# Optimization experiments

Measured on AMD Instinct MI355X. Metric: run time of the kernel, lower is better.

Reference implementation:

```python
import jax, jax.numpy as jnp
import numpy as np

B, S, H = 2, 2048, 4096
NH, HD = 32, 128          # num attention heads, head dim (kv_channels)
KVH = 2                   # multi_query_group_num (KV heads)
ROT = HD // 2             # 64 rotary dims -> rope cache last-2 dim = 32
QKV = NH * HD + 2 * KVH * HD  # 4608


def apply_rope(x, rope):
    # x: [b, nh, s, hd]; rope: [b, s, ROT//2, 2]
    b, nh, s, hd = x.shape
    x_rot, x_pass = x[..., :ROT], x[..., ROT:]
    xs = x_rot.reshape(b, nh, s, ROT // 2, 2)
    rc = rope[:, :s].reshape(b, 1, s, ROT // 2, 2)
    out = jnp.stack([
        xs[..., 0] * rc[..., 0] - xs[..., 1] * rc[..., 1],
        xs[..., 1] * rc[..., 0] + xs[..., 0] * rc[..., 1],
    ], axis=-1).reshape(b, nh, s, ROT)
    return jnp.concatenate([out, x_pass], axis=-1)


def setup_inputs() -> dict:
    key = jax.random.key(0)
    ks = jax.random.split(key, 6)
    hidden_states = jax.random.normal(ks[0], (B, S, H), dtype=jnp.float32)
    rotary_pos_emb = jax.random.normal(ks[1], (B, S, ROT // 2, 2), dtype=jnp.float32)
    # causal mask: True = masked (strict upper triangle), matching module's ~tril
    causal = jnp.triu(jnp.ones((S, S), dtype=jnp.bool_), k=1)
    attention_mask = jnp.broadcast_to(causal[None, None], (B, 1, S, S))
    W_qkv = jax.random.normal(ks[2], (QKV, H), dtype=jnp.float32) * (1.0 / np.sqrt(H))
    b_qkv = jax.random.normal(ks[3], (QKV,), dtype=jnp.float32) * 0.02
    W_dense = jax.random.normal(ks[4], (H, NH * HD), dtype=jnp.float32) * (1.0 / np.sqrt(NH * HD))
    return {"hidden_states": hidden_states, "rotary_pos_emb": rotary_pos_emb,
            "attention_mask": attention_mask, "W_qkv": W_qkv, "b_qkv": b_qkv,
            "W_dense": W_dense}


def reference(hidden_states, rotary_pos_emb, attention_mask, W_qkv, b_qkv, W_dense):
    b, s, _ = hidden_states.shape
    mixed = hidden_states @ W_qkv.T + b_qkv  # [b, s, QKV]
    q, k, v = jnp.split(mixed, [NH * HD, NH * HD + KVH * HD], axis=-1)
    q = q.reshape(b, s, NH, HD).transpose(0, 2, 1, 3)   # [b, NH, s, hd]
    k = k.reshape(b, s, KVH, HD).transpose(0, 2, 1, 3)  # [b, KVH, s, hd]
    v = v.reshape(b, s, KVH, HD).transpose(0, 2, 1, 3)
    q = apply_rope(q, rotary_pos_emb)
    k = apply_rope(k, rotary_pos_emb)
    # GQA expand KV heads to NH
    rep = NH // KVH
    k = jnp.repeat(k, rep, axis=1)
    v = jnp.repeat(v, rep, axis=1)
    scale = 1.0 / np.sqrt(HD)
    scores = jnp.einsum('bhqd,bhkd->bhqk', q, k).astype(jnp.float32) * scale
    scores = jnp.where(attention_mask, -jnp.inf, scores)
    probs = jax.nn.softmax(scores, axis=-1).astype(v.dtype)
    ctx = jnp.einsum('bhqk,bhkd->bhqd', probs, v)       # [b, NH, s, hd]
    ctx = ctx.transpose(0, 2, 1, 3).reshape(b, s, NH * HD)
    return ctx @ W_dense.T
```

## Files before the change

### kernel.cpp

```cpp
#include <hip/hip_runtime.h>
#include <hip/hip_bf16.h>
#include <stdint.h>

#define Bb 2
#define Ss 2048
#define Hh 4096
#define NHh 32
#define HDd 128
#define KVHh 2

typedef __attribute__((ext_vector_type(8))) short bf16x8;
typedef __attribute__((ext_vector_type(4))) float f32x4;
typedef __attribute__((ext_vector_type(16))) float f32x16;
typedef __attribute__((ext_vector_type(4))) unsigned int u32x4;
typedef unsigned short u16;
typedef unsigned int u32;
typedef unsigned long long u64;

__device__ __forceinline__ u16 f2b(float f) {
  union { float f; u32 u; } v; v.f = f;
  u32 r = v.u + 0x7fffu + ((v.u >> 16) & 1u);
  return (u16)(r >> 16);
}
__device__ __forceinline__ float b2f(u16 h) {
  union { u32 u; float f; } v; v.u = ((u32)h) << 16;
  return v.f;
}

__device__ __forceinline__ u32 cvtpk(float lo, float hi_) {
  u32 r;
  asm("v_cvt_pk_bf16_f32 %0, %1, %2" : "=v"(r) : "v"(lo), "v"(hi_));
  return r;
}
__device__ __forceinline__ void plswap(u32& x, u32& y) {
  asm volatile("v_permlane32_swap_b32 %0, %1" : "+v"(x), "+v"(y));
}

__device__ __forceinline__ void gload_lds16(const u16* g, u16* l) {
  __builtin_amdgcn_global_load_lds(
      (const __attribute__((address_space(1))) u32*)(uintptr_t)g,
      (__attribute__((address_space(3))) u32*)(u32)(uintptr_t)l,
      16, 0, 0);
}

__global__ void cvt_k(const float* __restrict__ in, u16* __restrict__ out, int n) {
  int i = blockIdx.x * blockDim.x + threadIdx.x;
  int idx = i * 4;
  if (idx >= n) return;
  float4 v = *(const float4*)&in[idx];
  u64 pack = (u64)f2b(v.x) | ((u64)f2b(v.y) << 16) |
             ((u64)f2b(v.z) << 32) | ((u64)f2b(v.w) << 48);
  *(u64*)&out[idx] = pack;
}

__global__ void rope_k(u16* __restrict__ X, const float* __restrict__ rope, int nheads) {
  int i = blockIdx.x * blockDim.x + threadIdx.x;
  int p = i & 31;
  int s = (i >> 5) & (Ss - 1);
  int bh = i >> 16;
  if (bh >= Bb * nheads) return;
  int b = bh / nheads;
  size_t base = ((size_t)bh * Ss + s) * HDd + p * 2;
  u32 x01 = *(u32*)&X[base];
  float x0 = b2f((u16)(x01 & 0xffff));
  float x1 = b2f((u16)(x01 >> 16));
  float2 rc = *(const float2*)&rope[(((size_t)b * Ss + s) * 32 + p) * 2];
  float o0 = x0 * rc.x - x1 * rc.y;
  float o1 = x1 * rc.x + x0 * rc.y;
  u32 o = (u32)f2b(o0) | ((u32)f2b(o1) << 16);
  *(u32*)&X[base] = o;
}

template <int KK>
__device__ __forceinline__ void stage_tileA(const u16* __restrict__ gbase, u16* dst, int tid) {
#pragma unroll
  for (int li = 0; li < 2; ++li) {
    int t16 = li * 512 + tid;
    int rt = t16 >> 2, ct = t16 & 3;
    int cg = ct ^ ((rt >> 1) & 3);
    gload_lds16(gbase + (size_t)rt * KK + cg * 8, dst + t16 * 8);
  }
}
template <int KK>
__device__ __forceinline__ void stage_tileB(const u16* __restrict__ gbase, u16* dst, int tid) {
  int t16 = tid;
  int rt = t16 >> 2, ct = t16 & 3;
  int cg = ct ^ ((rt >> 1) & 3);
  gload_lds16(gbase + (size_t)rt * KK + cg * 8, dst + t16 * 8);
}

__device__ __forceinline__ bf16x8 frag128(const u16* buf, int row, int lk) {
  int ch = lk ^ ((row >> 1) & 3);
  return *(const bf16x8*)&buf[row * 32 + ch * 8];
}

template <int NN, int KK, int COLG, int EPI>
__global__ __launch_bounds__(512, 4) void gemm256x128(
    const u16* __restrict__ A, const u16* __restrict__ Bm,
    float* __restrict__ Cout, const float* __restrict__ bias,
    u16* __restrict__ Qb, u16* __restrict__ Kb, u16* __restrict__ Vb) {
  __shared__ u16 As[2][8192];
  __shared__ u16 Bs[2][4096];
  const int tid = threadIdx.x;
  const int wave = tid >> 6;
  const int lane = tid & 63;
  const int lr = lane & 15;
  const int lk = lane >> 4;
  const int wr = wave >> 1;
  const int wc = wave & 1;
  const int bid = blockIdx.x;
  const int xcd = bid & 7;
  const int local = bid >> 3;
  const int rlr = local / COLG;
  const int rlc = local - rlr * COLG;
  const int m0 = ((xcd >> 2) * 8 + rlr) * 256;
  const int n0 = ((xcd & 3) * COLG + rlc) * 128;
  const int NT = KK / 32;

  f32x4 acc[4][4];
#pragma unroll
  for (int i = 0; i < 4; ++i)
#pragma unroll
    for (int j = 0; j < 4; ++j) acc[i][j] = (f32x4){0.f, 0.f, 0.f, 0.f};

  const u16* Ab = A + (size_t)m0 * KK;
  const u16* Bb_ = Bm + (size_t)n0 * KK;

  stage_tileA<KK>(Ab, &As[0][0], tid);
  stage_tileB<KK>(Bb_, &Bs[0][0], tid);
  asm volatile("s_waitcnt vmcnt(0)");
  __syncthreads();

  int cur = 0;
  for (int t = 0; t < NT; ++t) {
    if (t + 1 < NT) {
      stage_tileA<KK>(Ab + (t + 1) * 32, &As[cur ^ 1][0], tid);
      stage_tileB<KK>(Bb_ + (t + 1) * 32, &Bs[cur ^ 1][0], tid);
      asm volatile("s_waitcnt vmcnt(3)");
    } else {
      asm volatile("s_waitcnt vmcnt(0)");
    }
    __builtin_amdgcn_s_barrier();
    __builtin_amdgcn_sched_barrier(0);

    bf16x8 af[4], bf[4];
#pragma unroll
    for (int mi = 0; mi < 4; ++mi)
      af[mi] = frag128(&As[cur][0], wr * 64 + mi * 16 + lr, lk);
#pragma unroll
    for (int ni = 0; ni < 4; ++ni)
      bf[ni] = frag128(&Bs[cur][0], wc * 64 + ni * 16 + lr, lk);
    asm volatile("s_waitcnt lgkmcnt(0)");
    __builtin_amdgcn_sched_barrier(0);
    __builtin_amdgcn_s_setprio(1);
#pragma unroll
    for (int mi = 0; mi < 4; ++mi)
#pragma unroll
      for (int ni = 0; ni < 4; ++ni)
        acc[mi][ni] = __builtin_amdgcn_mfma_f32_16x16x32_bf16(af[mi], bf[ni], acc[mi][ni], 0, 0, 0);
    __builtin_amdgcn_s_setprio(0);
    __builtin_amdgcn_s_barrier();
    cur ^= 1;
  }

  if constexpr (EPI == 0) {
#pragma unroll
    for (int mi = 0; mi < 4; ++mi)
#pragma unroll
      for (int ni = 0; ni < 4; ++ni) {
        int col = n0 + wc * 64 + ni * 16 + lr;
        int rowb = m0 + wr * 64 + mi * 16 + lk * 4;
#pragma unroll
        for (int j = 0; j < 4; ++j)
          Cout[(size_t)(rowb + j) * NN + col] = acc[mi][ni][j];
      }
  } else {
#pragma unroll
    for (int ni = 0; ni < 4; ++ni) {
      int n = n0 + wc * 64 + ni * 16 + lr;
      float bv = bias[n];
#pragma unroll
      for (int mi = 0; mi < 4; ++mi) {
        int mb = m0 + wr * 64 + mi * 16 + lk * 4;
#pragma unroll
        for (int j = 0; j < 4; ++j) {
          int m = mb + j;
          int bb = m >> 11;
          int ss = m & 2047;
          u16 hv = f2b(acc[mi][ni][j] + bv);
          if (n < 4096) {
            Qb[(((size_t)bb * NHh + (n >> 7)) * Ss + ss) * HDd + (n & 127)] = hv;
          } else if (n < 4352) {
            int idx2 = n - 4096;
            Kb[(((size_t)bb * KVHh + (idx2 >> 7)) * Ss + ss) * HDd + (idx2 & 127)] = hv;
          } else {
            int idx2 = n - 4352;
            Vb[(((size_t)bb * KVHh + (idx2 >> 7)) * Ss + ss) * HDd + (idx2 & 127)] = hv;
          }
        }
      }
    }
  }
}

__global__ __launch_bounds__(512, 2) void attn_k(
    const u16* __restrict__ Qb, const u16* __restrict__ Kb,
    const u16* __restrict__ Vb, u16* __restrict__ Ctx) {
  __shared__ u16 Kt[2][64 * 128];
  __shared__ u16 Vt[2][128 * 64];
  const int tid = threadIdx.x;
  const int w = tid >> 6;
  const int lane = tid & 63;
  const int l31 = lane & 31;
  const int hi = lane >> 5;
  const int h = blockIdx.y, b = blockIdx.z;
  const int hkv = h >> 4;
  const u16* Qp = Qb + ((size_t)(b * NHh + h)) * Ss * HDd;
  const u16* Kp = Kb + ((size_t)(b * KVHh + hkv)) * Ss * HDd;
  const u16* Vp = Vb + ((size_t)(b * KVHh + hkv)) * Ss * HDd;

  const float scale = 0.08838834764831845f;
  const float L2E = 1.4426950408889634f;

  for (int hp = 0; hp < 2; ++hp) {
    const int qt = hp == 0 ? (7 - (int)blockIdx.x) : (int)blockIdx.x;
    const int qs = qt * 256;
    const int qw = qs + w * 32;
    const int qrow = qw + l31;
    const int nt = qs / 64 + 4;

    bf16x8 qf[8];
#pragma unroll
    for (int ds = 0; ds < 8; ++ds)
      qf[ds] = *(const bf16x8*)&Qp[(size_t)qrow * HDd + ds * 16 + hi * 8];

    f32x16 accO[4];
#pragma unroll
    for (int i = 0; i < 4; ++i)
#pragma unroll
      for (int r = 0; r < 16; ++r) accO[i][r] = 0.f;
    float m_r = -3.0e38f, l_r = 0.f;

    {
#pragma unroll
      for (int i = 0; i < 2; ++i) {
        int slot = w * 2 + i;
        int r = slot * 4 + (lane >> 4);
        int p = lane & 15;
        int gc = (p & 8) | ((p ^ r) & 7);
        gload_lds16(Kp + (size_t)r * HDd + gc * 8, &Kt[0][slot * 512]);
      }
      bf16x8 v0 = *(const bf16x8*)&Vp[(size_t)lane * HDd + w * 16];
      bf16x8 v1 = *(const bf16x8*)&Vp[(size_t)lane * HDd + w * 16 + 8];
      u32x4 sv = __builtin_bit_cast(u32x4, (lane & 1) ? v0 : v1);
      u32x4 rv;
      rv.x = __shfl_xor(sv.x, 1); rv.y = __shfl_xor(sv.y, 1);
      rv.z = __shfl_xor(sv.z, 1); rv.w = __shfl_xor(sv.w, 1);
      bf16x8 recv = __builtin_bit_cast(bf16x8, rv);
      int kvp = lane >> 1;
#pragma unroll
      for (int i = 0; i < 8; ++i) {
        int d = w * 16 + (lane & 1) * 8 + i;
        u16 lo = (lane & 1) ? (u16)recv[i] : (u16)v0[i];
        u16 hb = (lane & 1) ? (u16)v1[i] : (u16)recv[i];
        u32 val = (u32)lo | ((u32)hb << 16);
        int cp = (kvp >> 2) ^ (d & 7);
        *(u32*)&Vt[0][d * 64 + cp * 8 + (kvp & 3) * 2] = val;
      }
    }
    __syncthreads();

    for (int t = 0; t < nt; ++t) {
      const int j0 = t * 64;
      const int cur = t & 1;
      const bool havenext = (t + 1 < nt);
      bf16x8 nv0, nv1;
      if (havenext) {
        const int j1 = j0 + 64;
#pragma unroll
        for (int i = 0; i < 2; ++i) {
          int slot = w * 2 + i;
          int r = slot * 4 + (lane >> 4);
          int p = lane & 15;
          int gc = (p & 8) | ((p ^ r) & 7);
          gload_lds16(Kp + (size_t)(j1 + r) * HDd + gc * 8, &Kt[cur ^ 1][slot * 512]);
        }
        nv0 = *(const bf16x8*)&Vp[(size_t)(j1 + lane) * HDd + w * 16];
        nv1 = *(const bf16x8*)&Vp[(size_t)(j1 + lane) * HDd + w * 16 + 8];
      }

      if (j0 <= qw + 31) {
        f32x16 aS[2];
#pragma unroll
        for (int a = 0; a < 2; ++a)
#pragma unroll
          for (int r = 0; r < 16; ++r) aS[a][r] = 0.f;
#pragma unroll
        for (int kvb = 0; kvb < 2; ++kvb) {
          int r = kvb * 32 + l31;
#pragma unroll
          for (int ds = 0; ds < 8; ++ds) {
            int c = ds * 2 + hi;
            int cp = (c & 8) | ((c ^ r) & 7);
            bf16x8 kf = *(const bf16x8*)&Kt[cur][r * 128 + cp * 8];
            aS[kvb] = __builtin_amdgcn_mfma_f32_32x32x16_bf16(kf, qf[ds], aS[kvb], 0, 0, 0);
          }
        }
        const bool needmask = (j0 + 63 > qw);
        float mx = -3.0e38f;
#pragma unroll
        for (int a = 0; a < 2; ++a)
#pragma unroll
          for (int r = 0; r < 16; ++r) {
            float s = aS[a][r] * scale;
            if (needmask) {
              int kv = j0 + a * 32 + (r & 3) + 8 * (r >> 2) + 4 * hi;
              s = (kv > qrow) ? -3.0e38f : s;
            }
            aS[a][r] = s;
            mx = fmaxf(mx, s);
          }
        mx = fmaxf(mx, __shfl_xor(mx, 32));
        float mnew = fmaxf(m_r, mx);
        float corr = __builtin_amdgcn_exp2f((m_r - mnew) * L2E);
        float sum = 0.f;
#pragma unroll
        for (int a = 0; a < 2; ++a)
#pragma unroll
          for (int r = 0; r < 16; ++r) {
            float pe = __builtin_amdgcn_exp2f((aS[a][r] - mnew) * L2E);
            aS[a][r] = pe;
            sum += pe;
          }
        sum += __shfl_xor(sum, 32);
        l_r = l_r * corr + sum;
        m_r = mnew;
#pragma unroll
        for (int i = 0; i < 4; ++i)
#pragma unroll
          for (int r = 0; r < 16; ++r) accO[i][r] *= corr;

        u32 cc0[2][4], cc1[2][4];
#pragma unroll
        for (int a = 0; a < 2; ++a)
#pragma unroll
          for (int g = 0; g < 4; ++g) {
            cc0[a][g] = cvtpk(aS[a][g * 4 + 0], aS[a][g * 4 + 1]);
            cc1[a][g] = cvtpk(aS[a][g * 4 + 2], aS[a][g * 4 + 3]);
          }
        bf16x8 pa[4];
#pragma unroll
        for (int ks = 0; ks < 4; ++ks) {
          int a = ks >> 1, g0 = (ks & 1) * 2;
          u32 w0 = cc0[a][g0], w2 = cc0[a][g0 + 1];
          u32 w1 = cc1[a][g0], w3 = cc1[a][g0 + 1];
          plswap(w0, w2);
          plswap(w1, w3);
          u32x4 tv; tv.x = w0; tv.y = w1; tv.z = w2; tv.w = w3;
          pa[ks] = __builtin_bit_cast(bf16x8, tv);
        }
#pragma unroll
        for (int dblk = 0; dblk < 4; ++dblk) {
          int d = dblk * 32 + l31;
#pragma unroll
          for (int ks = 0; ks < 4; ++ks) {
            int c = ks * 2 + hi;
            int cp = c ^ (d & 7);
            bf16x8 vf = *(const bf16x8*)&Vt[cur][d * 64 + cp * 8];
            accO[dblk] = __builtin_amdgcn_mfma_f32_32x32x16_bf16(vf, pa[ks], accO[dblk], 0, 0, 0);
          }
        }
      }

      if (havenext) {
        u32x4 sv = __builtin_bit_cast(u32x4, (lane & 1) ? nv0 : nv1);
        u32x4 rv;
        rv.x = __shfl_xor(sv.x, 1); rv.y = __shfl_xor(sv.y, 1);
        rv.z = __shfl_xor(sv.z, 1); rv.w = __shfl_xor(sv.w, 1);
        bf16x8 recv = __builtin_bit_cast(bf16x8, rv);
        int kvp = lane >> 1;
#pragma unroll
        for (int i = 0; i < 8; ++i) {
          int d = w * 16 + (lane & 1) * 8 + i;
          u16 lo = (lane & 1) ? (u16)recv[i] : (u16)nv0[i];
          u16 hb = (lane & 1) ? (u16)nv1[i] : (u16)recv[i];
          u32 val = (u32)lo | ((u32)hb << 16);
          int cp = (kvp >> 2) ^ (d & 7);
          *(u32*)&Vt[cur ^ 1][d * 64 + cp * 8 + (kvp & 3) * 2] = val;
        }
      }
      __syncthreads();
    }

    {
      float il = 1.0f / l_r;
      size_t rb = ((size_t)b * Ss + qrow) * (size_t)(NHh * HDd) + (size_t)h * HDd;
#pragma unroll
      for (int dblk = 0; dblk < 4; ++dblk)
#pragma unroll
        for (int g = 0; g < 4; ++g) {
          int d0 = dblk * 32 + g * 8 + hi * 4;
          u64 pack = (u64)f2b(accO[dblk][g * 4 + 0] * il) |
                     ((u64)f2b(accO[dblk][g * 4 + 1] * il) << 16) |
                     ((u64)f2b(accO[dblk][g * 4 + 2] * il) << 32) |
                     ((u64)f2b(accO[dblk][g * 4 + 3] * il) << 48);
          *(u64*)&Ctx[rb + d0] = pack;
        }
    }
    __syncthreads();
  }
}

extern "C" void kernel_launch(void* const* d_in, const int* in_sizes, int n_in,
                              void* d_out, int out_size, void* d_ws, size_t ws_size,
                              hipStream_t stream) {
  const float* hidden = (const float*)d_in[0];
  const float* rope = (const float*)d_in[1];
  const float* Wqkv = (const float*)d_in[3];
  const float* bqkv = (const float*)d_in[4];
  const float* Wdense = (const float*)d_in[5];
  float* out = (float*)d_out;

  char* w = (char*)d_ws;
  u16* Xbf = (u16*)w;
  u16* ctx = Xbf;
  w += (size_t)33554432;
  u16* Wq = (u16*)w;
  u16* Wd = Wq;
  w += (size_t)37748736;
  u16* Qb = (u16*)w; w += (size_t)33554432;
  u16* Kb = (u16*)w; w += (size_t)2097152;
  u16* Vb = (u16*)w; w += (size_t)2097152;

  cvt_k<<<(16777216 / 4 + 255) / 256, 256, 0, stream>>>(hidden, Xbf, 16777216);
  cvt_k<<<(18874368 / 4 + 255) / 256, 256, 0, stream>>>(Wqkv, Wq, 18874368);
  gemm256x128<4608, 4096, 9, 1><<<dim3(576), 512, 0, stream>>>(
      Xbf, Wq, nullptr, bqkv, Qb, Kb, Vb);
  rope_k<<<(Bb * NHh * Ss * 32 + 255) / 256, 256, 0, stream>>>(Qb, rope, NHh);
  rope_k<<<(Bb * KVHh * Ss * 32 + 255) / 256, 256, 0, stream>>>(Kb, rope, KVHh);
  cvt_k<<<(16777216 / 4 + 255) / 256, 256, 0, stream>>>(Wdense, Wd, 16777216);
  attn_k<<<dim3(4, NHh, Bb), 512, 0, stream>>>(Qb, Kb, Vb, ctx);
  gemm256x128<4096, 4096, 8, 0><<<dim3(512), 512, 0, stream>>>(
      ctx, Wd, out, nullptr, nullptr, nullptr, nullptr);
}
```

Baseline: 510.9 us.

## Fuse RoPE into QKV GEMM epilogue, merge conversions, add lazy softmax rescale

Applies rotary embedding directly in the QKV GEMM epilogue using a lane shuffle to fetch the paired element, removing two separate rope passes over Q and K. Merges the three fp32-to-bf16 conversion launches into one kernel with a dedicated buffer for the dense weights. In attention, skips the running-max correction and accumulator rescale unless the max grows by more than a threshold, cutting per-tile multiply work at the cost of larger unnormalized exponentials.

```diff
diff --git a/kernel.cpp b/kernel.cpp
--- a/kernel.cpp
+++ b/kernel.cpp
@@ -43,32 +43,21 @@
       16, 0, 0);
 }
 
-__global__ void cvt_k(const float* __restrict__ in, u16* __restrict__ out, int n) {
+__global__ void cvt3_k(const float* __restrict__ a, u16* __restrict__ oa,
+                       const float* __restrict__ b, u16* __restrict__ ob,
+                       const float* __restrict__ c, u16* __restrict__ oc) {
   int i = blockIdx.x * blockDim.x + threadIdx.x;
-  int idx = i * 4;
-  if (idx >= n) return;
-  float4 v = *(const float4*)&in[idx];
+  const float* src;
+  u16* dst;
+  int off;
+  if (i < 4194304) { src = a; dst = oa; off = i; }
+  else if (i < 8912896) { src = b; dst = ob; off = i - 4194304; }
+  else { src = c; dst = oc; off = i - 8912896; }
+  int idx = off * 4;
+  float4 v = *(const float4*)&src[idx];
   u64 pack = (u64)f2b(v.x) | ((u64)f2b(v.y) << 16) |
              ((u64)f2b(v.z) << 32) | ((u64)f2b(v.w) << 48);
-  *(u64*)&out[idx] = pack;
-}
-
-__global__ void rope_k(u16* __restrict__ X, const float* __restrict__ rope, int nheads) {
-  int i = blockIdx.x * blockDim.x + threadIdx.x;
-  int p = i & 31;
-  int s = (i >> 5) & (Ss - 1);
-  int bh = i >> 16;
-  if (bh >= Bb * nheads) return;
-  int b = bh / nheads;
-  size_t base = ((size_t)bh * Ss + s) * HDd + p * 2;
-  u32 x01 = *(u32*)&X[base];
-  float x0 = b2f((u16)(x01 & 0xffff));
-  float x1 = b2f((u16)(x01 >> 16));
-  float2 rc = *(const float2*)&rope[(((size_t)b * Ss + s) * 32 + p) * 2];
-  float o0 = x0 * rc.x - x1 * rc.y;
-  float o1 = x1 * rc.x + x0 * rc.y;
-  u32 o = (u32)f2b(o0) | ((u32)f2b(o1) << 16);
-  *(u32*)&X[base] = o;
+  *(u64*)&dst[idx] = pack;
 }
 
 template <int KK>
@@ -98,6 +87,7 @@
 __global__ __launch_bounds__(512, 4) void gemm256x128(
     const u16* __restrict__ A, const u16* __restrict__ Bm,
     float* __restrict__ Cout, const float* __restrict__ bias,
+    const float* __restrict__ rope,
     u16* __restrict__ Qb, u16* __restrict__ Kb, u16* __restrict__ Vb) {
   __shared__ u16 As[2][8192];
   __shared__ u16 Bs[2][4096];
@@ -179,6 +169,10 @@
     for (int ni = 0; ni < 4; ++ni) {
       int n = n0 + wc * 64 + ni * 16 + lr;
       float bv = bias[n];
+      int d = n & 127;
+      int p = d >> 1;
+      bool isrot = (d < 64) && (n < 4352);
+      bool odd = (n & 1);
 #pragma unroll
       for (int mi = 0; mi < 4; ++mi) {
         int mb = m0 + wr * 64 + mi * 16 + lk * 4;
@@ -187,7 +181,13 @@
           int m = mb + j;
           int bb = m >> 11;
           int ss = m & 2047;
-          u16 hv = f2b(acc[mi][ni][j] + bv);
+          float v = acc[mi][ni][j] + bv;
+          float vv = __shfl_xor(v, 1);
+          if (isrot) {
+            float2 rc = *(const float2*)&rope[(((size_t)bb * Ss + ss) * 32 + p) * 2];
+            v = odd ? (v * rc.x + vv * rc.y) : (v * rc.x - vv * rc.y);
+          }
+          u16 hv = f2b(v);
           if (n < 4096) {
             Qb[(((size_t)bb * NHh + (n >> 7)) * Ss + ss) * HDd + (n & 127)] = hv;
           } else if (n < 4352) {
@@ -321,24 +321,27 @@
             mx = fmaxf(mx, s);
           }
         mx = fmaxf(mx, __shfl_xor(mx, 32));
-        float mnew = fmaxf(m_r, mx);
-        float corr = __builtin_amdgcn_exp2f((m_r - mnew) * L2E);
+        if (!__all(mx - m_r <= 8.0f)) {
+          float mnew = fmaxf(m_r, mx);
+          float corr = __builtin_amdgcn_exp2f((m_r - mnew) * L2E);
+          l_r *= corr;
+#pragma unroll
+          for (int i = 0; i < 4; ++i)
+#pragma unroll
+            for (int r = 0; r < 16; ++r) accO[i][r] *= corr;
+          m_r = mnew;
+        }
         float sum = 0.f;
 #pragma unroll
         for (int a = 0; a < 2; ++a)
 #pragma unroll
           for (int r = 0; r < 16; ++r) {
-            float pe = __builtin_amdgcn_exp2f((aS[a][r] - mnew) * L2E);
+            float pe = __builtin_amdgcn_exp2f((aS[a][r] - m_r) * L2E);
             aS[a][r] = pe;
             sum += pe;
           }
         sum += __shfl_xor(sum, 32);
-        l_r = l_r * corr + sum;
-        m_r = mnew;
-#pragma unroll
-        for (int i = 0; i < 4; ++i)
-#pragma unroll
-          for (int r = 0; r < 16; ++r) accO[i][r] *= corr;
+        l_r += sum;
 
         u32 cc0[2][4], cc1[2][4];
 #pragma unroll
@@ -425,21 +428,16 @@
   u16* Xbf = (u16*)w;
   u16* ctx = Xbf;
   w += (size_t)33554432;
-  u16* Wq = (u16*)w;
-  u16* Wd = Wq;
-  w += (size_t)37748736;
+  u16* Wq = (u16*)w; w += (size_t)37748736;
+  u16* Wd = (u16*)w; w += (size_t)33554432;
   u16* Qb = (u16*)w; w += (size_t)33554432;
   u16* Kb = (u16*)w; w += (size_t)2097152;
   u16* Vb = (u16*)w; w += (size_t)2097152;
 
-  cvt_k<<<(16777216 / 4 + 255) / 256, 256, 0, stream>>>(hidden, Xbf, 16777216);
-  cvt_k<<<(18874368 / 4 + 255) / 256, 256, 0, stream>>>(Wqkv, Wq, 18874368);
+  cvt3_k<<<51200, 256, 0, stream>>>(hidden, Xbf, Wqkv, Wq, Wdense, Wd);
   gemm256x128<4608, 4096, 9, 1><<<dim3(576), 512, 0, stream>>>(
-      Xbf, Wq, nullptr, bqkv, Qb, Kb, Vb);
-  rope_k<<<(Bb * NHh * Ss * 32 + 255) / 256, 256, 0, stream>>>(Qb, rope, NHh);
-  rope_k<<<(Bb * KVHh * Ss * 32 + 255) / 256, 256, 0, stream>>>(Kb, rope, KVHh);
-  cvt_k<<<(16777216 / 4 + 255) / 256, 256, 0, stream>>>(Wdense, Wd, 16777216);
+      Xbf, Wq, nullptr, bqkv, rope, Qb, Kb, Vb);
   attn_k<<<dim3(4, NHh, Bb), 512, 0, stream>>>(Qb, Kb, Vb, ctx);
   gemm256x128<4096, 4096, 8, 0><<<dim3(512), 512, 0, stream>>>(
-      ctx, Wd, out, nullptr, nullptr, nullptr, nullptr);
-}
+      ctx, Wd, out, nullptr, nullptr, nullptr, nullptr, nullptr);
+}
```

Result: no change. 512.5 us (+0.3%).
